# Optimization experiments

Hardware: AMD Instinct MI355X
Metric: run time of the kernel (lower is better)

The kernel has to match this reference:

```python
import jax, jax.numpy as jnp
import numpy as np

N_ATOMS = 512
ATOM_SHAPE = (3, 3, 3)
SPARSE_ITERS = 128
FPB = 8  # features_per_band


def unit_norm(x, axis=-1, eps=1e-12):
    n = jnp.linalg.norm(x, axis=axis, keepdims=True)
    return x / jnp.maximum(n, eps)


def best_fit(signal, atoms):
    # signal: [B, bands, time, per] ; atoms: [n_atoms, 3,3,3]
    B, bands, time, per = signal.shape
    sig = signal[:, None]  # [B,1,bands,time,per]
    # pad (0,2) on last three dims
    sig = jnp.pad(sig, ((0, 0), (0, 0), (0, 2), (0, 2), (0, 2)))
    # conv3d correlation: lax conv with NCDHW / OIDHW
    fm = jax.lax.conv_general_dilated(
        sig, atoms[:, None], window_strides=(1, 1, 1), padding='VALID',
        dimension_numbers=('NCDHW', 'OIDHW', 'NCDHW'))  # [B, n_atoms, bands, time, per]
    flat = fm.reshape(B, -1)
    idx = jnp.argmax(flat, axis=-1)
    val = jnp.take_along_axis(flat, idx[:, None], axis=-1)[:, 0]
    # unflatten index -> (atom, b, c, d)
    fshape = fm.shape[1:]
    a_i = idx // (fshape[1] * fshape[2] * fshape[3])
    rem = idx % (fshape[1] * fshape[2] * fshape[3])
    b_i = rem // (fshape[2] * fshape[3])
    rem = rem % (fshape[2] * fshape[3])
    c_i = rem // fshape[3]
    d_i = rem % fshape[3]

    def per_batch(sig_b, a, b, c, dd, v):
        # sig_b: padded [bands+2, time+2, per+2]
        atom = atoms[a] * v  # [3,3,3]
        # Since conv output spatial extent = input extent (valid over padded),
        # max offsets b,c,d <= dims-1 of padded-2, slice always fits fully.
        patch = jax.lax.dynamic_slice(sig_b, (b, c, dd), ATOM_SHAPE)
        return jax.lax.dynamic_update_slice(sig_b, patch - atom, (b, c, dd))

    sig2 = jax.vmap(per_batch)(sig[:, 0], a_i, b_i, c_i, d_i, val)
    return sig2[:, :bands, :time, :per]


def sparse_code(signal, atoms):
    def body(res, _):
        return best_fit(res, atoms), None
    res, _ = jax.lax.scan(body, signal, None, length=SPARSE_ITERS)
    return res


def layer_norm(x, g, b, eps=1e-5):
    m = jnp.mean(x, axis=-1, keepdims=True)
    v = jnp.var(x, axis=-1, keepdims=True)
    return (x - m) / jnp.sqrt(v + eps) * g + b


def batch_norm(x, g, b, eps=1e-5):
    # x: [B, C, T]; training-mode batch stats over (B, T)
    m = jnp.mean(x, axis=(0, 2), keepdims=True)
    v = jnp.var(x, axis=(0, 2), keepdims=True)
    return (x - m) / jnp.sqrt(v + eps) * g[None, :, None] + b[None, :, None]


def conv1d(x, w, b, pad):
    # x: [B,C,T], w: [O,I,K]
    y = jax.lax.conv_general_dilated(x, w, (1,), [(pad, pad)],
                                     dimension_numbers=('NCT', 'OIT', 'NCT'))
    return y + b[None, :, None]


def upsample4(x):
    # nearest, scale 4 along time
    return jnp.repeat(x, 4, axis=-1)


def setup_inputs() -> dict:
    key = jax.random.key(0)
    ks = jax.random.split(key, 24)
    w = 0.05
    x = jax.random.normal(ks[0], (4, 128, 128, 257), dtype=jnp.float32)
    d = jax.random.uniform(ks[1], (N_ATOMS, 27), minval=-1, maxval=1)
    atoms = unit_norm(d, axis=-1).reshape(N_ATOMS, *ATOM_SHAPE)
    inp = {
        'x': x,
        'atoms': atoms,
        'embed_w': jax.random.normal(ks[2], (257, FPB)) * w,
        'embed_b': jnp.zeros((FPB,)),
        # LinearOutputStack(1024, 3, out 1024, LayerNorm): 3 hidden-ish linears
        'ctx_w1': jax.random.normal(ks[3], (1024, 1024)) * w,
        'ctx_b1': jnp.zeros((1024,)),
        'ctx_g1': jnp.ones((1024,)), 'ctx_be1': jnp.zeros((1024,)),
        'ctx_w2': jax.random.normal(ks[4], (1024, 1024)) * w,
        'ctx_b2': jnp.zeros((1024,)),
        'ctx_g2': jnp.ones((1024,)), 'ctx_be2': jnp.zeros((1024,)),
        'ctx_w3': jax.random.normal(ks[5], (1024, 1024)) * w,
        'ctx_b3': jnp.zeros((1024,)),
        # up stack conv weights
        'up_w1': jax.random.normal(ks[6], (512, 1024, 7)) * w,
        'up_b1': jnp.zeros((512,)), 'bn_g1': jnp.ones((512,)), 'bn_b1': jnp.zeros((512,)),
        'up_w2': jax.random.normal(ks[7], (256, 512, 7)) * w,
        'up_b2': jnp.zeros((256,)), 'bn_g2': jnp.ones((256,)), 'bn_b2': jnp.zeros((256,)),
        'up_w3': jax.random.normal(ks[8], (128, 256, 7)) * w,
        'up_b3': jnp.zeros((128,)), 'bn_g3': jnp.ones((128,)), 'bn_b3': jnp.zeros((128,)),
        'up_w4': jax.random.normal(ks[9], (64, 128, 7)) * w,
        'up_b4': jnp.zeros((64,)), 'bn_g4': jnp.ones((64,)), 'bn_b4': jnp.zeros((64,)),
        'up_w5': jax.random.normal(ks[10], (1, 64, 7)) * w,
        'up_b5': jnp.zeros((1,)),
    }
    return inp


def reference(x, atoms, embed_w, embed_b,
              ctx_w1, ctx_b1, ctx_g1, ctx_be1,
              ctx_w2, ctx_b2, ctx_g2, ctx_be2,
              ctx_w3, ctx_b3,
              up_w1, up_b1, bn_g1, bn_b1,
              up_w2, up_b2, bn_g2, bn_b2,
              up_w3, up_b3, bn_g3, bn_b3,
              up_w4, up_b4, bn_g4, bn_b4,
              up_w5, up_b5):
    B, bands, time, per = x.shape
    # embed_features
    e = x @ embed_w + embed_b  # [B, bands, time, 8]
    # sparse coding (no_grad in original; result discarded but computed)
    _res = jax.lax.stop_gradient(sparse_code(e, atoms))
    encoded = jnp.transpose(e, (0, 3, 1, 2)).reshape(B, FPB * bands, time)  # [B,1024,T]
    # context
    ctx = jnp.sum(encoded, axis=-1)  # [B,1024]
    h = layer_norm(jax.nn.leaky_relu(ctx @ ctx_w1 + ctx_b1, 0.2), ctx_g1, ctx_be1)
    h = layer_norm(jax.nn.leaky_relu(h @ ctx_w2 + ctx_b2, 0.2), ctx_g2, ctx_be2)
    ctx_out = h @ ctx_w3 + ctx_b3
    # generate (up stack)
    y = jax.nn.leaky_relu(batch_norm(conv1d(encoded, up_w1, up_b1, 3), bn_g1, bn_b1), 0.2)
    y = upsample4(y)
    y = jax.nn.leaky_relu(batch_norm(conv1d(y, up_w2, up_b2, 3), bn_g2, bn_b2), 0.2)
    y = upsample4(y)
    y = jax.nn.leaky_relu(batch_norm(conv1d(y, up_w3, up_b3, 3), bn_g3, bn_b3), 0.2)
    y = upsample4(y)
    y = jax.nn.leaky_relu(batch_norm(conv1d(y, up_w4, up_b4, 3), bn_g4, bn_b4), 0.2)
    y = upsample4(y)
    y = conv1d(y, up_w5, up_b5, 3)  # [B,1,T*256]
    # reverb approximated as identity mix (ReverbGenerator source unavailable)
    return y, ctx_out
```

## Files before the change

kernel.cpp:

```cpp
#include <hip/hip_runtime.h>
#include <hip/hip_bf16.h>

using sh8   = __attribute__((ext_vector_type(8))) short;
using f32x4 = __attribute__((ext_vector_type(4))) float;

#define DEV __device__ __forceinline__

DEV float leaky(float x) { return x >= 0.f ? x : 0.2f * x; }

DEV unsigned short f2bf(float f) {
  unsigned u = __float_as_uint(f);
  u += 0x7FFF + ((u >> 16) & 1);
  return (unsigned short)(u >> 16);
}
DEV float bf2f(unsigned short b) { return __uint_as_float(((unsigned)b) << 16); }

template<int Cout, int Cin>
DEV void pack7_body(const float* __restrict__ w, unsigned short* __restrict__ wp, int blk) {
  constexpr long plane = (long)(Cin >> 5) * Cout * 32;
  int tid = blk * 256 + threadIdx.x;
  if (tid >= Cout * Cin) return;
  int co = tid / Cin, ci = tid - co * Cin;
  const float* src = w + (long)tid * 7;
  unsigned short* dst = wp + ((long)(ci >> 5) * Cout + co) * 32 + (ci & 31);
  #pragma unroll
  for (int k = 0; k < 7; ++k) dst[k * plane] = f2bf(src[k]);
}
template<int Cout, int Cin>
DEV void packph_body(const float* __restrict__ w, unsigned short* __restrict__ wp, int blk) {
  constexpr long plane = (long)(Cin >> 5) * Cout * 32;
  int tid = blk * 256 + threadIdx.x;
  if (tid >= Cout * Cin) return;
  int co = tid / Cin, ci = tid - co * Cin;
  float wk[7];
  #pragma unroll
  for (int k = 0; k < 7; ++k) wk[k] = w[(long)tid * 7 + k];
  unsigned short* dst = wp + ((long)(ci >> 5) * Cout + co) * 32 + (ci & 31);
  #pragma unroll
  for (int p = 0; p < 4; ++p) {
    #pragma unroll
    for (int d = 0; d < 3; ++d) {
      float s = 0.f;
      #pragma unroll
      for (int k = 0; k < 7; ++k) if (((p + k + 1) >> 2) == d) s += wk[k];
      dst[(p * 3 + d) * plane] = f2bf(s);
    }
  }
}
__global__ __launch_bounds__(256)
void pack_all(const float* __restrict__ w1, const float* __restrict__ w2,
              const float* __restrict__ w3, const float* __restrict__ w4,
              unsigned short* __restrict__ wbuf) {
  int blk = blockIdx.x;
  if (blk < 2048)      pack7_body<512, 1024>(w1, wbuf, blk);
  else if (blk < 2560) packph_body<256, 512>(w2, wbuf + 3670016, blk - 2048);
  else if (blk < 2688) packph_body<128, 256>(w3, wbuf + 5242880, blk - 2560);
  else                 packph_body<64, 128>(w4, wbuf + 5636096, blk - 2688);
}

__global__ __launch_bounds__(256)
void embed_mfma(const float* __restrict__ x, const float* __restrict__ ew,
                const float* __restrict__ eb, unsigned short* __restrict__ encbf,
                float* __restrict__ part) {
  __shared__ unsigned short W16[257 * 16];
  __shared__ float ctxred[4][8];
  const int tid = threadIdx.x;

  for (int i = tid; i < 257 * 16; i += 256) {
    int p = i >> 4, f = i & 15;
    W16[i] = (f < 8) ? f2bf(ew[p * 8 + f]) : (unsigned short)0;
  }
  __syncthreads();

  const int w = tid >> 6, lane = tid & 63;
  const int m = lane & 15, g = lane >> 4;

  sh8 breg[8];
  #pragma unroll
  for (int kk = 0; kk < 8; ++kk) {
    #pragma unroll
    for (int j = 0; j < 8; ++j)
      breg[kk][j] = (short)W16[(kk * 32 + g * 8 + j) * 16 + m];
  }
  const float w256 = bf2f(W16[256 * 16 + m]);
  const float ebf = (m < 8) ? eb[m] : 0.f;

  const int bid = blockIdx.x;
  const long row0 = (long)bid * 64;
  const int b = bid >> 8, band = (bid >> 1) & 127, half = bid & 1;
  const int t0 = half * 64 + w * 16;

  const float* xp = x + (row0 + w * 16 + m) * 257 + g * 8;
  float vals[8][8];
  #pragma unroll
  for (int kk = 0; kk < 8; ++kk) {
    #pragma unroll
    for (int j = 0; j < 8; ++j)
      vals[kk][j] = xp[kk * 32 + j];
  }
  f32x4 acc = {0.f, 0.f, 0.f, 0.f};
  #pragma unroll
  for (int kk = 0; kk < 8; ++kk) {
    sh8 afr;
    #pragma unroll
    for (int j = 0; j < 8; ++j) afr[j] = (short)f2bf(vals[kk][j]);
    acc = __builtin_amdgcn_mfma_f32_16x16x32_bf16(afr, breg[kk], acc, 0, 0, 0);
  }

  const float* xq = x + (row0 + w * 16 + g * 4) * 257 + 256;
  float ctx_acc = 0.f;
  unsigned short pk[4];
  #pragma unroll
  for (int r = 0; r < 4; ++r) {
    float e = acc[r] + xq[(long)r * 257] * w256 + ebf;
    pk[r] = f2bf(e);
    ctx_acc += e;
  }
  if (m < 8) {
    long o = ((long)b * 1024 + m * 128 + band) * 128 + t0 + g * 4;
    *(ushort4*)(encbf + o) = make_ushort4(pk[0], pk[1], pk[2], pk[3]);
  }

  ctx_acc += __shfl_xor(ctx_acc, 16);
  ctx_acc += __shfl_xor(ctx_acc, 32);
  if (lane < 8) ctxred[w][lane] = ctx_acc;
  __syncthreads();
  if (tid < 8) {
    float sv = ctxred[0][tid] + ctxred[1][tid] + ctxred[2][tid] + ctxred[3][tid];
    part[((b * 1024 + tid * 128 + band) << 1) + half] = sv;
  }
}

template<int SUM2>
__global__ void gemm_p(const float* __restrict__ h, const float* __restrict__ w,
                       float* __restrict__ gpart) {
  __shared__ float hl[4][128];
  __shared__ float red[8][4][32];
  const int kc = blockIdx.y, jb = blockIdx.x, k0 = kc * 128;
  for (int i = threadIdx.x; i < 512; i += 256) {
    int bb = i >> 7, kk = i & 127;
    float v;
    if (SUM2) {
      int base = ((bb << 10) + k0 + kk) << 1;
      v = h[base] + h[base + 1];
    } else {
      v = h[(bb << 10) + k0 + kk];
    }
    hl[bb][kk] = v;
  }
  __syncthreads();
  const int jl = threadIdx.x & 31, kq = threadIdx.x >> 5;
  const int j = jb * 32 + jl;
  float a0 = 0, a1 = 0, a2 = 0, a3 = 0;
  const float* wp = w + (long)(k0 + kq * 16) * 1024 + j;
  #pragma unroll
  for (int k = 0; k < 16; ++k) {
    float wv = wp[(long)k * 1024];
    a0 += hl[0][kq * 16 + k] * wv;
    a1 += hl[1][kq * 16 + k] * wv;
    a2 += hl[2][kq * 16 + k] * wv;
    a3 += hl[3][kq * 16 + k] * wv;
  }
  red[kq][0][jl] = a0; red[kq][1][jl] = a1; red[kq][2][jl] = a2; red[kq][3][jl] = a3;
  __syncthreads();
  if (threadIdx.x < 128) {
    int bb = threadIdx.x >> 5, j2 = threadIdx.x & 31;
    float s = 0;
    #pragma unroll
    for (int q = 0; q < 8; ++q) s += red[q][bb][j2];
    gpart[((long)kc * 4 + bb) * 1024 + jb * 32 + j2] = s;
  }
}

__global__ void lnsum_kernel(const float* __restrict__ gpart, const float* __restrict__ bias,
                             const float* __restrict__ g, const float* __restrict__ be,
                             float* __restrict__ out) {
  int b = blockIdx.x;
  __shared__ float buf[1024];
  __shared__ float rs[4], rq[4];
  float s = 0, q = 0;
  #pragma unroll
  for (int i = 0; i < 4; ++i) {
    int j = threadIdx.x + i * 256;
    float v = bias[j];
    #pragma unroll
    for (int kc = 0; kc < 8; ++kc) v += gpart[((long)kc * 4 + b) * 1024 + j];
    v = leaky(v);
    buf[j] = v; s += v; q += v * v;
  }
  #pragma unroll
  for (int off = 32; off; off >>= 1) { s += __shfl_down(s, off); q += __shfl_down(q, off); }
  int wid = threadIdx.x >> 6, lane = threadIdx.x & 63;
  if (lane == 0) { rs[wid] = s; rq[wid] = q; }
  __syncthreads();
  float S = rs[0] + rs[1] + rs[2] + rs[3];
  float Q = rq[0] + rq[1] + rq[2] + rq[3];
  float mean = S * (1.f / 1024.f);
  float var = Q * (1.f / 1024.f) - mean * mean;
  float rstd = rsqrtf(var + 1e-5f);
  #pragma unroll
  for (int i = 0; i < 4; ++i) {
    int j = threadIdx.x + i * 256;
    out[b * 1024 + j] = (buf[j] - mean) * rstd * g[j] + be[j];
  }
}

__global__ void fin_kernel(const float* __restrict__ gpart, const float* __restrict__ bias,
                           float* __restrict__ out) {
  int i = blockIdx.x * 256 + threadIdx.x;
  int b = i >> 10, j = i & 1023;
  float v = bias[j];
  #pragma unroll
  for (int kc = 0; kc < 8; ++kc) v += gpart[((long)kc * 4 + b) * 1024 + j];
  out[i] = v;
}

template<int UPS, int SPLITK>
__global__ __launch_bounds__(256, 2)
void conv_mfma(const unsigned short* __restrict__ act,
               const unsigned short* __restrict__ wpack,
               float* __restrict__ outp,
               int Cin, int Cout, int Tout) {
  constexpr int NC = (UPS == 1) ? 70 : 18;
  const int Tin = Tout / UPS;
  const int cpb = Cin / SPLITK;
  const int ncib = cpb >> 5;
  const int nCibTot = Cin >> 5;
  const int nco = Cout >> 6, nt = Tout >> 6;

  int bid = blockIdx.x;
  const int sk = bid % SPLITK; bid /= SPLITK;
  const int tt = bid % nt;  bid /= nt;
  const int cot = bid % nco; bid /= nco;
  const int b = bid;
  const int t0 = tt << 6, co0 = cot << 6;
  const int ci0 = sk * cpb;

  extern __shared__ unsigned short lin[];

  const unsigned short* actb = act + ((long)b * Cin + ci0) * Tin;
  const int u_base = (UPS == 1) ? (t0 - 3) : ((t0 >> 2) - 1);
  const int total = cpb * NC;
  for (int i = threadIdx.x; i < total; i += 256) {
    int ci = i / NC, ul = i - ci * NC;
    int u = u_base + ul;
    unsigned short v = 0;
    if (u >= 0 && u < Tin) v = actb[(long)ci * Tin + u];
    lin[((ci >> 5) * NC + ul) * 40 + (ci & 31)] = v;
  }
  __syncthreads();

  const int lane = threadIdx.x & 63, w = threadIdx.x >> 6;
  const int m = lane & 15, g = lane >> 4;

  int boff[28];
  #pragma unroll
  for (int s = 0; s < 4; ++s) {
    #pragma unroll
    for (int k = 0; k < 7; ++k) {
      int row = (UPS == 1) ? (s * 16 + m + k)
                           : (s * 4 + ((m + k + 9) >> 2) - 2);
      boff[s * 7 + k] = row * 40 + g * 8;
    }
  }

  const long wlane = ((long)(co0 + w * 16 + m) * 4 + g) * 8;

  f32x4 acc[4];
  #pragma unroll
  for (int s = 0; s < 4; ++s) { acc[s][0] = 0.f; acc[s][1] = 0.f; acc[s][2] = 0.f; acc[s][3] = 0.f; }

  for (int cib = 0; cib < ncib; ++cib) {
    const unsigned short* lb = lin + cib * (NC * 40);
    const int cg = (ci0 >> 5) + cib;
    sh8 a[7];
    #pragma unroll
    for (int k = 0; k < 7; ++k)
      a[k] = *(const sh8*)(wpack + (long)(k * nCibTot + cg) * Cout * 32 + wlane);
    #pragma unroll
    for (int k = 0; k < 7; ++k) {
      #pragma unroll
      for (int s = 0; s < 4; ++s) {
        sh8 bfr = *(const sh8*)(lb + boff[s * 7 + k]);
        acc[s] = __builtin_amdgcn_mfma_f32_16x16x32_bf16(a[k], bfr, acc[s], 0, 0, 0);
      }
    }
  }

  float* op = outp + (((long)sk * 4 + b) * Cout + (co0 + w * 16 + g * 4)) * (long)Tout + t0 + m;
  #pragma unroll
  for (int r = 0; r < 4; ++r) {
    #pragma unroll
    for (int s = 0; s < 4; ++s)
      op[(long)r * Tout + s * 16] = acc[s][r];
  }
}

template<int SPLITK>
__global__ __launch_bounds__(256, 2)
void conv_ph(const float* __restrict__ csum_in, const float* __restrict__ sp,
             const float* __restrict__ g, const float* __restrict__ be,
             const unsigned short* __restrict__ wpack,
             float* __restrict__ outp,
             int Cin, int Cout, int Tin) {
  const int Tout = Tin << 2;
  const int cpb = Cin / SPLITK;
  const int ncib = cpb >> 5;
  const int nCibTot = Cin >> 5;
  const int nco = Cout >> 6, ntu = Tin >> 6;

  int bid = blockIdx.x;
  const int sk = bid % SPLITK; bid /= SPLITK;
  const int tu = bid % ntu; bid /= ntu;
  const int cot = bid % nco; bid /= nco;
  const int b = bid;
  const int u0 = tu << 6, co0 = cot << 6;
  const int ci0 = sk * cpb;

  extern __shared__ unsigned short lin[];
  __shared__ float ssc[64], ssh[64];

  if (threadIdx.x < cpb) {
    int c = ci0 + threadIdx.x;
    float S = sp[c * 4] + sp[c * 4 + 1] + sp[c * 4 + 2] + sp[c * 4 + 3];
    float Q = sp[Cin * 4 + c * 4] + sp[Cin * 4 + c * 4 + 1] + sp[Cin * 4 + c * 4 + 2] + sp[Cin * 4 + c * 4 + 3];
    float n = 4.f * (float)Tin;
    float mean = S / n;
    float var = Q / n - mean * mean;
    float sc = g[c] * rsqrtf(var + 1e-5f);
    ssc[threadIdx.x] = sc;
    ssh[threadIdx.x] = be[c] - mean * sc;
  }
  __syncthreads();

  const float* csb = csum_in + ((long)b * Cin + ci0) * Tin;
  const int total = cpb * 66;
  for (int i = threadIdx.x; i < total; i += 256) {
    int ci = i / 66, r = i - ci * 66;
    int u = u0 - 1 + r;
    unsigned short v = 0;
    if (u >= 0 && u < Tin) {
      float t = csb[(long)ci * Tin + u];
      v = f2bf(leaky(t * ssc[ci] + ssh[ci]));
    }
    lin[((ci >> 5) * 66 + r) * 40 + (ci & 31)] = v;
  }
  __syncthreads();

  const int lane = threadIdx.x & 63, w = threadIdx.x >> 6;
  const int m = lane & 15, g2 = lane >> 4;

  int boff[4][3];
  #pragma unroll
  for (int s = 0; s < 4; ++s)
    #pragma unroll
    for (int d = 0; d < 3; ++d)
      boff[s][d] = (s * 16 + m + d) * 40 + g2 * 8;

  const long wlane = ((long)(co0 + w * 16 + m)) * 32 + g2 * 8;

  f32x4 acc[4][4];
  #pragma unroll
  for (int s = 0; s < 4; ++s)
    #pragma unroll
    for (int p = 0; p < 4; ++p) { acc[s][p][0] = 0.f; acc[s][p][1] = 0.f; acc[s][p][2] = 0.f; acc[s][p][3] = 0.f; }

  for (int cib = 0; cib < ncib; ++cib) {
    const unsigned short* lb = lin + cib * (66 * 40);
    const int cg = (ci0 >> 5) + cib;
    sh8 a[12];
    #pragma unroll
    for (int pd = 0; pd < 12; ++pd)
      a[pd] = *(const sh8*)(wpack + ((long)(pd * nCibTot + cg) * Cout) * 32 + wlane);
    #pragma unroll
    for (int s = 0; s < 4; ++s) {
      sh8 b0 = *(const sh8*)(lb + boff[s][0]);
      sh8 b1 = *(const sh8*)(lb + boff[s][1]);
      sh8 b2 = *(const sh8*)(lb + boff[s][2]);
      acc[s][0] = __builtin_amdgcn_mfma_f32_16x16x32_bf16(a[0],  b0, acc[s][0], 0, 0, 0);
      acc[s][0] = __builtin_amdgcn_mfma_f32_16x16x32_bf16(a[1],  b1, acc[s][0], 0, 0, 0);
      acc[s][1] = __builtin_amdgcn_mfma_f32_16x16x32_bf16(a[3],  b0, acc[s][1], 0, 0, 0);
      acc[s][1] = __builtin_amdgcn_mfma_f32_16x16x32_bf16(a[4],  b1, acc[s][1], 0, 0, 0);
      acc[s][1] = __builtin_amdgcn_mfma_f32_16x16x32_bf16(a[5],  b2, acc[s][1], 0, 0, 0);
      acc[s][2] = __builtin_amdgcn_mfma_f32_16x16x32_bf16(a[6],  b0, acc[s][2], 0, 0, 0);
      acc[s][2] = __builtin_amdgcn_mfma_f32_16x16x32_bf16(a[7],  b1, acc[s][2], 0, 0, 0);
      acc[s][2] = __builtin_amdgcn_mfma_f32_16x16x32_bf16(a[8],  b2, acc[s][2], 0, 0, 0);
      acc[s][3] = __builtin_amdgcn_mfma_f32_16x16x32_bf16(a[10], b1, acc[s][3], 0, 0, 0);
      acc[s][3] = __builtin_amdgcn_mfma_f32_16x16x32_bf16(a[11], b2, acc[s][3], 0, 0, 0);
    }
  }

  float* op = outp + (((long)sk * 4 + b) * Cout + (co0 + w * 16 + g2 * 4)) * (long)Tout;
  #pragma unroll
  for (int r = 0; r < 4; ++r) {
    #pragma unroll
    for (int s = 0; s < 4; ++s) {
      float4 v4 = make_float4(acc[s][0][r], acc[s][1][r], acc[s][2][r], acc[s][3][r]);
      *(float4*)(op + (long)r * Tout + ((u0 + s * 16 + m) << 2)) = v4;
    }
  }
}

__global__ void bnsum_kernel(const float* __restrict__ p, float* __restrict__ sp,
                             float* __restrict__ csum, int C, int T, int SK) {
  int c = blockIdx.x, b = blockIdx.y;
  long stride = (long)4 * C * T;
  const float* r = p + ((long)b * C + c) * T;
  float* cw = csum + ((long)b * C + c) * T;
  float s = 0, q = 0;
  for (int t = threadIdx.x; t < T; t += 256) {
    float v = r[t];
    for (int k = 1; k < SK; ++k) v += r[t + k * stride];
    cw[t] = v;
    s += v; q += v * v;
  }
  #pragma unroll
  for (int off = 32; off; off >>= 1) { s += __shfl_down(s, off); q += __shfl_down(q, off); }
  __shared__ float rs[4], rq[4];
  int wid = threadIdx.x >> 6, lane = threadIdx.x & 63;
  if (lane == 0) { rs[wid] = s; rq[wid] = q; }
  __syncthreads();
  if (threadIdx.x == 0) {
    sp[c * 4 + b] = rs[0] + rs[1] + rs[2] + rs[3];
    sp[C * 4 + c * 4 + b] = rq[0] + rq[1] + rq[2] + rq[3];
  }
}

__global__ __launch_bounds__(256)
void conv5_kernel(const float* __restrict__ csum_in, const float* __restrict__ sp,
                  const float* __restrict__ g, const float* __restrict__ be,
                  const float* __restrict__ wgt, const float* __restrict__ bias,
                  float* __restrict__ out, int Tout) {
  __shared__ unsigned short sv[64 * 66];
  __shared__ float wph[64 * 13];
  __shared__ float ssc[64], ssh[64];

  const int b = blockIdx.y;
  const int u0 = blockIdx.x * 64;
  const int Tin = Tout >> 2;
  const int tid = threadIdx.x;

  {
    int ci = tid >> 2, pp = tid & 3;
    float s0 = 0, s1 = 0, s2 = 0;
    #pragma unroll
    for (int k = 0; k < 7; ++k) {
      int d = (pp - 3 + k + 4) >> 2;
      float wv = wgt[ci * 7 + k];
      if (d == 0) s0 += wv; else if (d == 1) s1 += wv; else s2 += wv;
    }
    wph[ci * 13 + pp * 3 + 0] = s0;
    wph[ci * 13 + pp * 3 + 1] = s1;
    wph[ci * 13 + pp * 3 + 2] = s2;
  }
  if (tid < 64) {
    float S = sp[tid * 4] + sp[tid * 4 + 1] + sp[tid * 4 + 2] + sp[tid * 4 + 3];
    float Q = sp[256 + tid * 4] + sp[256 + tid * 4 + 1] + sp[256 + tid * 4 + 2] + sp[256 + tid * 4 + 3];
    float n = 4.f * (float)Tin;
    float mean = S / n;
    float var = Q / n - mean * mean;
    float sc = g[tid] * rsqrtf(var + 1e-5f);
    ssc[tid] = sc;
    ssh[tid] = be[tid] - mean * sc;
  }
  __syncthreads();

  const float* inb = csum_in + (long)b * 64 * Tin;
  for (int i = tid; i < 64 * 66; i += 256) {
    int ci = i / 66, uu = i - ci * 66;
    int u = u0 - 1 + uu;
    unsigned short v = 0;
    if (u >= 0 && u < Tin) {
      float t = inb[(long)ci * Tin + u];
      v = f2bf(leaky(t * ssc[ci] + ssh[ci]));
    }
    sv[ci * 66 + uu] = v;
  }
  __syncthreads();

  const int ul = tid >> 2;
  const int chunk = tid & 3;
  float a0 = 0, a1 = 0, a2 = 0, a3 = 0;
  #pragma unroll
  for (int cc = 0; cc < 16; ++cc) {
    int ci = chunk * 16 + cc;
    float v0 = bf2f(sv[ci * 66 + ul]);
    float v1 = bf2f(sv[ci * 66 + ul + 1]);
    float v2 = bf2f(sv[ci * 66 + ul + 2]);
    const float* wp = wph + ci * 13;
    a0 += v0 * wp[0] + v1 * wp[1];
    a1 += v0 * wp[3] + v1 * wp[4] + v2 * wp[5];
    a2 += v0 * wp[6] + v1 * wp[7] + v2 * wp[8];
    a3 += v1 * wp[10] + v2 * wp[11];
  }
  #pragma unroll
  for (int msk = 1; msk <= 2; msk <<= 1) {
    a0 += __shfl_xor(a0, msk);
    a1 += __shfl_xor(a1, msk);
    a2 += __shfl_xor(a2, msk);
    a3 += __shfl_xor(a3, msk);
  }
  if (chunk == 0) {
    float bv = bias[0];
    float4 r = make_float4(a0 + bv, a1 + bv, a2 + bv, a3 + bv);
    *(float4*)(out + (long)b * Tout + (long)(u0 + ul) * 4) = r;
  }
}

extern "C" void kernel_launch(void* const* d_in, const int* in_sizes, int n_in,
                              void* d_out, int out_size, void* d_ws, size_t ws_size,
                              hipStream_t stream) {
  const float* x     = (const float*)d_in[0];
  const float* ew    = (const float*)d_in[2];
  const float* eb    = (const float*)d_in[3];
  const float* w1    = (const float*)d_in[4];
  const float* b1    = (const float*)d_in[5];
  const float* g1    = (const float*)d_in[6];
  const float* be1   = (const float*)d_in[7];
  const float* w2    = (const float*)d_in[8];
  const float* b2    = (const float*)d_in[9];
  const float* g2    = (const float*)d_in[10];
  const float* be2   = (const float*)d_in[11];
  const float* w3    = (const float*)d_in[12];
  const float* b3    = (const float*)d_in[13];
  const float* up_w1 = (const float*)d_in[14];
  const float* up_b1 = (const float*)d_in[15];
  const float* bn_g1 = (const float*)d_in[16];
  const float* bn_b1 = (const float*)d_in[17];
  const float* up_w2 = (const float*)d_in[18];
  const float* up_b2 = (const float*)d_in[19];
  const float* bn_g2 = (const float*)d_in[20];
  const float* bn_b2 = (const float*)d_in[21];
  const float* up_w3 = (const float*)d_in[22];
  const float* up_b3 = (const float*)d_in[23];
  const float* bn_g3 = (const float*)d_in[24];
  const float* bn_b3 = (const float*)d_in[25];
  const float* up_w4 = (const float*)d_in[26];
  const float* up_b4 = (const float*)d_in[27];
  const float* bn_g4 = (const float*)d_in[28];
  const float* bn_b4 = (const float*)d_in[29];
  const float* up_w5 = (const float*)d_in[30];
  const float* up_b5 = (const float*)d_in[31];

  float* out = (float*)d_out;

  float* ws = (float*)d_ws;
  float* part   = ws;
  float* gpart  = part + 8192;
  float* t2     = gpart + 32768;
  float* statsp = t2 + 4096;
  float* csum   = statsp + 4096;
  float* pbuf   = csum + 2097152;
  unsigned short* encbf = (unsigned short*)(pbuf + 4194304);
  unsigned short* wbuf  = encbf + 524288;

  pack_all<<<2720, 256, 0, stream>>>(up_w1, up_w2, up_w3, up_w4, wbuf);
  embed_mfma<<<1024, 256, 0, stream>>>(x, ew, eb, encbf, part);

  gemm_p<1><<<dim3(32, 8), 256, 0, stream>>>(part, w1, gpart);
  lnsum_kernel<<<4, 256, 0, stream>>>(gpart, b1, g1, be1, t2);
  gemm_p<0><<<dim3(32, 8), 256, 0, stream>>>(t2, w2, gpart);
  lnsum_kernel<<<4, 256, 0, stream>>>(gpart, b2, g2, be2, t2);
  gemm_p<0><<<dim3(32, 8), 256, 0, stream>>>(t2, w3, gpart);
  fin_kernel<<<16, 256, 0, stream>>>(gpart, b3, out + 131072);

  conv_mfma<1, 8><<<512, 256, 22400, stream>>>(encbf, wbuf, pbuf, 1024, 512, 128);
  bnsum_kernel<<<dim3(512, 4), 256, 0, stream>>>(pbuf, statsp, csum, 512, 128, 8);

  conv_ph<8><<<256, 256, 10560, stream>>>(csum, statsp, bn_g1, bn_b1, wbuf + 3670016, pbuf, 512, 256, 128);
  bnsum_kernel<<<dim3(256, 4), 256, 0, stream>>>(pbuf, statsp, csum, 256, 512, 8);

  conv_ph<4><<<256, 256, 10560, stream>>>(csum, statsp, bn_g2, bn_b2, wbuf + 5242880, pbuf, 256, 128, 512);
  bnsum_kernel<<<dim3(128, 4), 256, 0, stream>>>(pbuf, statsp, csum, 128, 2048, 4);

  conv_ph<2><<<256, 256, 10560, stream>>>(csum, statsp, bn_g3, bn_b3, wbuf + 5636096, pbuf, 128, 64, 2048);
  bnsum_kernel<<<dim3(64, 4), 256, 0, stream>>>(pbuf, statsp, csum, 64, 8192, 2);

  conv5_kernel<<<dim3(128, 4), 256, 0, stream>>>(csum, statsp, bn_g4, bn_b4, up_w5, up_b5, out, 32768);
}
```

Before: 168.5 us.

## Merge context MLP kernels into conv and batchnorm launches via extra blocks

The weight-pack kernel is merged into the embed kernel, and the context MLP stages are folded into the conv and bnsum launches as extra trailing blocks. The GEMM blocks run inside the conv kernels and the LayerNorm/final-sum blocks run inside the bnsum kernels. This cuts the launch count from about 18 to 10 and lets the small MLP work overlap with the conv pipeline. In exchange, the fused kernels carry extra shared memory and registers from the merged bodies, which may affect occupancy.

```diff
diff --git a/kernel.cpp b/kernel.cpp
--- a/kernel.cpp
+++ b/kernel.cpp
@@ -47,100 +47,16 @@
     }
   }
 }
-__global__ __launch_bounds__(256)
-void pack_all(const float* __restrict__ w1, const float* __restrict__ w2,
-              const float* __restrict__ w3, const float* __restrict__ w4,
-              unsigned short* __restrict__ wbuf) {
-  int blk = blockIdx.x;
-  if (blk < 2048)      pack7_body<512, 1024>(w1, wbuf, blk);
-  else if (blk < 2560) packph_body<256, 512>(w2, wbuf + 3670016, blk - 2048);
-  else if (blk < 2688) packph_body<128, 256>(w3, wbuf + 5242880, blk - 2560);
-  else                 packph_body<64, 128>(w4, wbuf + 5636096, blk - 2688);
-}
-
-__global__ __launch_bounds__(256)
-void embed_mfma(const float* __restrict__ x, const float* __restrict__ ew,
-                const float* __restrict__ eb, unsigned short* __restrict__ encbf,
-                float* __restrict__ part) {
-  __shared__ unsigned short W16[257 * 16];
-  __shared__ float ctxred[4][8];
-  const int tid = threadIdx.x;
-
-  for (int i = tid; i < 257 * 16; i += 256) {
-    int p = i >> 4, f = i & 15;
-    W16[i] = (f < 8) ? f2bf(ew[p * 8 + f]) : (unsigned short)0;
-  }
-  __syncthreads();
-
-  const int w = tid >> 6, lane = tid & 63;
-  const int m = lane & 15, g = lane >> 4;
-
-  sh8 breg[8];
-  #pragma unroll
-  for (int kk = 0; kk < 8; ++kk) {
-    #pragma unroll
-    for (int j = 0; j < 8; ++j)
-      breg[kk][j] = (short)W16[(kk * 32 + g * 8 + j) * 16 + m];
-  }
-  const float w256 = bf2f(W16[256 * 16 + m]);
-  const float ebf = (m < 8) ? eb[m] : 0.f;
-
-  const int bid = blockIdx.x;
-  const long row0 = (long)bid * 64;
-  const int b = bid >> 8, band = (bid >> 1) & 127, half = bid & 1;
-  const int t0 = half * 64 + w * 16;
-
-  const float* xp = x + (row0 + w * 16 + m) * 257 + g * 8;
-  float vals[8][8];
-  #pragma unroll
-  for (int kk = 0; kk < 8; ++kk) {
-    #pragma unroll
-    for (int j = 0; j < 8; ++j)
-      vals[kk][j] = xp[kk * 32 + j];
-  }
-  f32x4 acc = {0.f, 0.f, 0.f, 0.f};
-  #pragma unroll
-  for (int kk = 0; kk < 8; ++kk) {
-    sh8 afr;
-    #pragma unroll
-    for (int j = 0; j < 8; ++j) afr[j] = (short)f2bf(vals[kk][j]);
-    acc = __builtin_amdgcn_mfma_f32_16x16x32_bf16(afr, breg[kk], acc, 0, 0, 0);
-  }
-
-  const float* xq = x + (row0 + w * 16 + g * 4) * 257 + 256;
-  float ctx_acc = 0.f;
-  unsigned short pk[4];
-  #pragma unroll
-  for (int r = 0; r < 4; ++r) {
-    float e = acc[r] + xq[(long)r * 257] * w256 + ebf;
-    pk[r] = f2bf(e);
-    ctx_acc += e;
-  }
-  if (m < 8) {
-    long o = ((long)b * 1024 + m * 128 + band) * 128 + t0 + g * 4;
-    *(ushort4*)(encbf + o) = make_ushort4(pk[0], pk[1], pk[2], pk[3]);
-  }
-
-  ctx_acc += __shfl_xor(ctx_acc, 16);
-  ctx_acc += __shfl_xor(ctx_acc, 32);
-  if (lane < 8) ctxred[w][lane] = ctx_acc;
-  __syncthreads();
-  if (tid < 8) {
-    float sv = ctxred[0][tid] + ctxred[1][tid] + ctxred[2][tid] + ctxred[3][tid];
-    part[((b * 1024 + tid * 128 + band) << 1) + half] = sv;
-  }
-}
-
-template<int SUM2>
-__global__ void gemm_p(const float* __restrict__ h, const float* __restrict__ w,
-                       float* __restrict__ gpart) {
+
+DEV void gemm_body(int gb, const float* __restrict__ h, const float* __restrict__ w,
+                   float* __restrict__ gpart, int sum2) {
   __shared__ float hl[4][128];
   __shared__ float red[8][4][32];
-  const int kc = blockIdx.y, jb = blockIdx.x, k0 = kc * 128;
+  const int jb = gb & 31, kc = gb >> 5, k0 = kc * 128;
   for (int i = threadIdx.x; i < 512; i += 256) {
     int bb = i >> 7, kk = i & 127;
     float v;
-    if (SUM2) {
+    if (sum2) {
       int base = ((bb << 10) + k0 + kk) << 1;
       v = h[base] + h[base + 1];
     } else {
@@ -172,55 +88,99 @@
   }
 }
 
-__global__ void lnsum_kernel(const float* __restrict__ gpart, const float* __restrict__ bias,
-                             const float* __restrict__ g, const float* __restrict__ be,
-                             float* __restrict__ out) {
-  int b = blockIdx.x;
-  __shared__ float buf[1024];
-  __shared__ float rs[4], rq[4];
-  float s = 0, q = 0;
-  #pragma unroll
-  for (int i = 0; i < 4; ++i) {
-    int j = threadIdx.x + i * 256;
-    float v = bias[j];
-    #pragma unroll
-    for (int kc = 0; kc < 8; ++kc) v += gpart[((long)kc * 4 + b) * 1024 + j];
-    v = leaky(v);
-    buf[j] = v; s += v; q += v * v;
-  }
-  #pragma unroll
-  for (int off = 32; off; off >>= 1) { s += __shfl_down(s, off); q += __shfl_down(q, off); }
-  int wid = threadIdx.x >> 6, lane = threadIdx.x & 63;
-  if (lane == 0) { rs[wid] = s; rq[wid] = q; }
-  __syncthreads();
-  float S = rs[0] + rs[1] + rs[2] + rs[3];
-  float Q = rq[0] + rq[1] + rq[2] + rq[3];
-  float mean = S * (1.f / 1024.f);
-  float var = Q * (1.f / 1024.f) - mean * mean;
-  float rstd = rsqrtf(var + 1e-5f);
-  #pragma unroll
-  for (int i = 0; i < 4; ++i) {
-    int j = threadIdx.x + i * 256;
-    out[b * 1024 + j] = (buf[j] - mean) * rstd * g[j] + be[j];
-  }
-}
-
-__global__ void fin_kernel(const float* __restrict__ gpart, const float* __restrict__ bias,
-                           float* __restrict__ out) {
-  int i = blockIdx.x * 256 + threadIdx.x;
-  int b = i >> 10, j = i & 1023;
-  float v = bias[j];
-  #pragma unroll
-  for (int kc = 0; kc < 8; ++kc) v += gpart[((long)kc * 4 + b) * 1024 + j];
-  out[i] = v;
+__global__ __launch_bounds__(256)
+void embed_pack(const float* __restrict__ x, const float* __restrict__ ew,
+                const float* __restrict__ eb, unsigned short* __restrict__ encbf,
+                float* __restrict__ part,
+                const float* __restrict__ cw1, const float* __restrict__ cw2,
+                const float* __restrict__ cw3, const float* __restrict__ cw4,
+                unsigned short* __restrict__ wbuf) {
+  if (blockIdx.x >= 1024) {
+    int blk = blockIdx.x - 1024;
+    if (blk < 2048)      pack7_body<512, 1024>(cw1, wbuf, blk);
+    else if (blk < 2560) packph_body<256, 512>(cw2, wbuf + 3670016, blk - 2048);
+    else if (blk < 2688) packph_body<128, 256>(cw3, wbuf + 5242880, blk - 2560);
+    else                 packph_body<64, 128>(cw4, wbuf + 5636096, blk - 2688);
+    return;
+  }
+  __shared__ unsigned short W16[257 * 16];
+  __shared__ float ctxred[4][8];
+  const int tid = threadIdx.x;
+
+  for (int i = tid; i < 257 * 16; i += 256) {
+    int p = i >> 4, f = i & 15;
+    W16[i] = (f < 8) ? f2bf(ew[p * 8 + f]) : (unsigned short)0;
+  }
+  __syncthreads();
+
+  const int w = tid >> 6, lane = tid & 63;
+  const int m = lane & 15, g = lane >> 4;
+
+  sh8 breg[8];
+  #pragma unroll
+  for (int kk = 0; kk < 8; ++kk) {
+    #pragma unroll
+    for (int j = 0; j < 8; ++j)
+      breg[kk][j] = (short)W16[(kk * 32 + g * 8 + j) * 16 + m];
+  }
+  const float w256 = bf2f(W16[256 * 16 + m]);
+  const float ebf = (m < 8) ? eb[m] : 0.f;
+
+  const int bid = blockIdx.x;
+  const long row0 = (long)bid * 64;
+  const int b = bid >> 8, band = (bid >> 1) & 127, half = bid & 1;
+  const int t0 = half * 64 + w * 16;
+
+  const float* xp = x + (row0 + w * 16 + m) * 257 + g * 8;
+  float vals[8][8];
+  #pragma unroll
+  for (int kk = 0; kk < 8; ++kk) {
+    #pragma unroll
+    for (int j = 0; j < 8; ++j)
+      vals[kk][j] = xp[kk * 32 + j];
+  }
+  f32x4 acc = {0.f, 0.f, 0.f, 0.f};
+  #pragma unroll
+  for (int kk = 0; kk < 8; ++kk) {
+    sh8 afr;
+    #pragma unroll
+    for (int j = 0; j < 8; ++j) afr[j] = (short)f2bf(vals[kk][j]);
+    acc = __builtin_amdgcn_mfma_f32_16x16x32_bf16(afr, breg[kk], acc, 0, 0, 0);
+  }
+
+  const float* xq = x + (row0 + w * 16 + g * 4) * 257 + 256;
+  float ctx_acc = 0.f;
+  unsigned short pk[4];
+  #pragma unroll
+  for (int r = 0; r < 4; ++r) {
+    float e = acc[r] + xq[(long)r * 257] * w256 + ebf;
+    pk[r] = f2bf(e);
+    ctx_acc += e;
+  }
+  if (m < 8) {
+    long o = ((long)b * 1024 + m * 128 + band) * 128 + t0 + g * 4;
+    *(ushort4*)(encbf + o) = make_ushort4(pk[0], pk[1], pk[2], pk[3]);
+  }
+
+  ctx_acc += __shfl_xor(ctx_acc, 16);
+  ctx_acc += __shfl_xor(ctx_acc, 32);
+  if (lane < 8) ctxred[w][lane] = ctx_acc;
+  __syncthreads();
+  if (tid < 8) {
+    float sv = ctxred[0][tid] + ctxred[1][tid] + ctxred[2][tid] + ctxred[3][tid];
+    part[((b * 1024 + tid * 128 + band) << 1) + half] = sv;
+  }
 }
 
 template<int UPS, int SPLITK>
 __global__ __launch_bounds__(256, 2)
-void conv_mfma(const unsigned short* __restrict__ act,
-               const unsigned short* __restrict__ wpack,
-               float* __restrict__ outp,
-               int Cin, int Cout, int Tout) {
+void conv_mfma_g(const unsigned short* __restrict__ act,
+                 const unsigned short* __restrict__ wpack,
+                 float* __restrict__ outp,
+                 int Cin, int Cout, int Tout, int nconv,
+                 const float* __restrict__ h, const float* __restrict__ wmlp,
+                 float* __restrict__ gpart, int sum2) {
+  if ((int)blockIdx.x >= nconv) { gemm_body(blockIdx.x - nconv, h, wmlp, gpart, sum2); return; }
   constexpr int NC = (UPS == 1) ? 70 : 18;
   const int Tin = Tout / UPS;
   const int cpb = Cin / SPLITK;
@@ -298,11 +258,14 @@
 
 template<int SPLITK>
 __global__ __launch_bounds__(256, 2)
-void conv_ph(const float* __restrict__ csum_in, const float* __restrict__ sp,
-             const float* __restrict__ g, const float* __restrict__ be,
-             const unsigned short* __restrict__ wpack,
-             float* __restrict__ outp,
-             int Cin, int Cout, int Tin) {
+void conv_ph_g(const float* __restrict__ csum_in, const float* __restrict__ sp,
+               const float* __restrict__ g, const float* __restrict__ be,
+               const unsigned short* __restrict__ wpack,
+               float* __restrict__ outp,
+               int Cin, int Cout, int Tin, int nconv,
+               const float* __restrict__ h, const float* __restrict__ wmlp,
+               float* __restrict__ gpart, int sum2) {
+  if ((int)blockIdx.x >= nconv) { gemm_body(blockIdx.x - nconv, h, wmlp, gpart, sum2); return; }
   const int Tout = Tin << 2;
   const int cpb = Cin / SPLITK;
   const int ncib = cpb >> 5;
@@ -401,9 +364,54 @@
   }
 }
 
-__global__ void bnsum_kernel(const float* __restrict__ p, float* __restrict__ sp,
-                             float* __restrict__ csum, int C, int T, int SK) {
-  int c = blockIdx.x, b = blockIdx.y;
+__global__ __launch_bounds__(256)
+void bnsum_ln(const float* __restrict__ p, float* __restrict__ sp,
+              float* __restrict__ csum, int C, int T, int SK, int mode,
+              const float* __restrict__ gpart, const float* __restrict__ bias,
+              const float* __restrict__ g, const float* __restrict__ be,
+              float* __restrict__ outp) {
+  const int nbn = C * 4;
+  if ((int)blockIdx.x >= nbn) {
+    if (mode == 1) {
+      int b = blockIdx.x - nbn;
+      __shared__ float buf[1024];
+      __shared__ float rs2[4], rq2[4];
+      float s = 0, q = 0;
+      #pragma unroll
+      for (int i = 0; i < 4; ++i) {
+        int j = threadIdx.x + i * 256;
+        float v = bias[j];
+        #pragma unroll
+        for (int kc = 0; kc < 8; ++kc) v += gpart[((long)kc * 4 + b) * 1024 + j];
+        v = leaky(v);
+        buf[j] = v; s += v; q += v * v;
+      }
+      #pragma unroll
+      for (int off = 32; off; off >>= 1) { s += __shfl_down(s, off); q += __shfl_down(q, off); }
+      int wid = threadIdx.x >> 6, lane = threadIdx.x & 63;
+      if (lane == 0) { rs2[wid] = s; rq2[wid] = q; }
+      __syncthreads();
+      float S = rs2[0] + rs2[1] + rs2[2] + rs2[3];
+      float Q = rq2[0] + rq2[1] + rq2[2] + rq2[3];
+      float mean = S * (1.f / 1024.f);
+      float var = Q * (1.f / 1024.f) - mean * mean;
+      float rstd = rsqrtf(var + 1e-5f);
+      #pragma unroll
+      for (int i = 0; i < 4; ++i) {
+        int j = threadIdx.x + i * 256;
+        outp[b * 1024 + j] = (buf[j] - mean) * rstd * g[j] + be[j];
+      }
+    } else {
+      int i = (blockIdx.x - nbn) * 256 + threadIdx.x;
+      int b = i >> 10, j = i & 1023;
+      float v = bias[j];
+      #pragma unroll
+      for (int kc = 0; kc < 8; ++kc) v += gpart[((long)kc * 4 + b) * 1024 + j];
+      outp[i] = v;
+    }
+    return;
+  }
+  const int c = blockIdx.x >> 2, b = blockIdx.x & 3;
   long stride = (long)4 * C * T;
   const float* r = p + ((long)b * C + c) * T;
   float* cw = csum + ((long)b * C + c) * T;
@@ -554,27 +562,27 @@
   unsigned short* encbf = (unsigned short*)(pbuf + 4194304);
   unsigned short* wbuf  = encbf + 524288;
 
-  pack_all<<<2720, 256, 0, stream>>>(up_w1, up_w2, up_w3, up_w4, wbuf);
-  embed_mfma<<<1024, 256, 0, stream>>>(x, ew, eb, encbf, part);
-
-  gemm_p<1><<<dim3(32, 8), 256, 0, stream>>>(part, w1, gpart);
-  lnsum_kernel<<<4, 256, 0, stream>>>(gpart, b1, g1, be1, t2);
-  gemm_p<0><<<dim3(32, 8), 256, 0, stream>>>(t2, w2, gpart);
-  lnsum_kernel<<<4, 256, 0, stream>>>(gpart, b2, g2, be2, t2);
-  gemm_p<0><<<dim3(32, 8), 256, 0, stream>>>(t2, w3, gpart);
-  fin_kernel<<<16, 256, 0, stream>>>(gpart, b3, out + 131072);
-
-  conv_mfma<1, 8><<<512, 256, 22400, stream>>>(encbf, wbuf, pbuf, 1024, 512, 128);
-  bnsum_kernel<<<dim3(512, 4), 256, 0, stream>>>(pbuf, statsp, csum, 512, 128, 8);
-
-  conv_ph<8><<<256, 256, 10560, stream>>>(csum, statsp, bn_g1, bn_b1, wbuf + 3670016, pbuf, 512, 256, 128);
-  bnsum_kernel<<<dim3(256, 4), 256, 0, stream>>>(pbuf, statsp, csum, 256, 512, 8);
-
-  conv_ph<4><<<256, 256, 10560, stream>>>(csum, statsp, bn_g2, bn_b2, wbuf + 5242880, pbuf, 256, 128, 512);
-  bnsum_kernel<<<dim3(128, 4), 256, 0, stream>>>(pbuf, statsp, csum, 128, 2048, 4);
-
-  conv_ph<2><<<256, 256, 10560, stream>>>(csum, statsp, bn_g3, bn_b3, wbuf + 5636096, pbuf, 128, 64, 2048);
-  bnsum_kernel<<<dim3(64, 4), 256, 0, stream>>>(pbuf, statsp, csum, 64, 8192, 2);
-
+  embed_pack<<<3744, 256, 0, stream>>>(x, ew, eb, encbf, part,
+                                       up_w1, up_w2, up_w3, up_w4, wbuf);
+
+  conv_mfma_g<1, 8><<<768, 256, 22400, stream>>>(encbf, wbuf, pbuf, 1024, 512, 128,
+                                                 512, part, w1, gpart, 1);
+  bnsum_ln<<<2052, 256, 0, stream>>>(pbuf, statsp, csum, 512, 128, 8, 1,
+                                     gpart, b1, g1, be1, t2);
+  conv_ph_g<8><<<512, 256, 10560, stream>>>(csum, statsp, bn_g1, bn_b1, wbuf + 3670016,
+                                            pbuf, 512, 256, 128,
+                                            256, t2, w2, gpart, 0);
+  bnsum_ln<<<1028, 256, 0, stream>>>(pbuf, statsp, csum, 256, 512, 8, 1,
+                                     gpart, b2, g2, be2, t2);
+  conv_ph_g<4><<<512, 256, 10560, stream>>>(csum, statsp, bn_g2, bn_b2, wbuf + 5242880,
+                                            pbuf, 256, 128, 512,
+                                            256, t2, w3, gpart, 0);
+  bnsum_ln<<<528, 256, 0, stream>>>(pbuf, statsp, csum, 128, 2048, 4, 2,
+                                    gpart, b3, b3, b3, out + 131072);
+  conv_ph_g<2><<<256, 256, 10560, stream>>>(csum, statsp, bn_g3, bn_b3, wbuf + 5636096,
+                                            pbuf, 128, 64, 2048,
+                                            256, t2, w3, gpart, -1);
+  bnsum_ln<<<256, 256, 0, stream>>>(pbuf, statsp, csum, 64, 8192, 2, 0,
+                                    gpart, b3, b3, b3, out + 131072);
   conv5_kernel<<<dim3(128, 4), 256, 0, stream>>>(csum, statsp, bn_g4, bn_b4, up_w5, up_b5, out, 32768);
 }
```

Measured after the change: 147.6 us. 12.4% less time.
